# Kernel tuning notes

Measured on AMD Instinct MI355X. Metric: run time of the kernel, lower is better.

The kernel has to match this reference:

```python
import jax, jax.numpy as jnp
import numpy as np

H = 1024      # hidden_size
NH = 16       # num_heads
HD = H // NH  # head_dim
MLP_DIM = 4096
EPS = 1e-6


def setup_inputs() -> dict:
    key = jax.random.key(0)
    ks = jax.random.split(key, 16)
    B, S = 8, 1024
    s_in = 1.0 / np.sqrt(H)
    s_mlp = 1.0 / np.sqrt(MLP_DIM)
    return {
        "x": jax.random.normal(ks[0], (B, S, H), jnp.float32),
        "ln1_g": jnp.ones((H,), jnp.float32),
        "ln1_b": jnp.zeros((H,), jnp.float32),
        "Wq": jax.random.normal(ks[1], (H, H), jnp.float32) * s_in,
        "bq": jnp.zeros((H,), jnp.float32),
        "Wk": jax.random.normal(ks[2], (H, H), jnp.float32) * s_in,
        "bk": jnp.zeros((H,), jnp.float32),
        "Wv": jax.random.normal(ks[3], (H, H), jnp.float32) * s_in,
        "bv": jnp.zeros((H,), jnp.float32),
        "Wo": jax.random.normal(ks[4], (H, H), jnp.float32) * s_in,
        "bo": jnp.zeros((H,), jnp.float32),
        "ln2_g": jnp.ones((H,), jnp.float32),
        "ln2_b": jnp.zeros((H,), jnp.float32),
        "W1": jax.random.normal(ks[5], (H, MLP_DIM), jnp.float32) * s_in,
        "b1": jnp.zeros((MLP_DIM,), jnp.float32),
        "W2": jax.random.normal(ks[6], (MLP_DIM, H), jnp.float32) * s_mlp,
        "b2": jnp.zeros((H,), jnp.float32),
    }


def _layernorm(x, g, b):
    mu = jnp.mean(x, axis=-1, keepdims=True)
    var = jnp.mean(jnp.square(x - mu), axis=-1, keepdims=True)
    return (x - mu) * jax.lax.rsqrt(var + EPS) * g + b


def reference(x, ln1_g, ln1_b, Wq, bq, Wk, bk, Wv, bv, Wo, bo,
              ln2_g, ln2_b, W1, b1, W2, b2):
    B, S, _ = x.shape
    # pre-LN attention
    h = _layernorm(x, ln1_g, ln1_b)
    q = (h @ Wq + bq).reshape(B, S, NH, HD).transpose(0, 2, 1, 3)  # bhsd
    k = (h @ Wk + bk).reshape(B, S, NH, HD).transpose(0, 2, 1, 3)
    v = (h @ Wv + bv).reshape(B, S, NH, HD).transpose(0, 2, 1, 3)
    scale = HD ** -0.5
    scores = jnp.einsum('bhqd,bhkd->bhqk', q, k) * scale
    weights = jax.nn.softmax(scores, axis=-1)
    attended = jnp.einsum('bhqk,bhkd->bhqd', weights, v)
    attended = attended.transpose(0, 2, 1, 3).reshape(B, S, H)
    x = x + attended @ Wo + bo
    # pre-LN MLP
    h = _layernorm(x, ln2_g, ln2_b)
    h = jax.nn.gelu(h @ W1 + b1, approximate=False)
    x = x + h @ W2 + b2
    return x
```

## Files before the change

kernel.cpp:

```cpp
#include <hip/hip_runtime.h>

#define H_DIM 1024
#define NHEADS 16
#define HD 64
#define SEQ 1024
#define BATCH 8
#define ROWS (BATCH*SEQ)
#define MLPD 4096

typedef __bf16 bf16x8 __attribute__((ext_vector_type(8)));
typedef float f32x4 __attribute__((ext_vector_type(4)));

__device__ __forceinline__ unsigned short f2bf(float f) {
    unsigned u = __float_as_uint(f);
    unsigned r = u + 0x7FFFu + ((u >> 16) & 1u);
    return (unsigned short)(r >> 16);
}

__global__ void transpose_w(const float* __restrict__ in, unsigned short* __restrict__ out,
                            int K, int N)
{
    __shared__ float tile[32][33];
    const int n0 = blockIdx.x * 32, k0 = blockIdx.y * 32;
    const int tx = threadIdx.x, ty = threadIdx.y;
    #pragma unroll
    for (int i = ty; i < 32; i += 8)
        tile[i][tx] = in[(size_t)(k0 + i) * N + n0 + tx];
    __syncthreads();
    #pragma unroll
    for (int i = ty; i < 32; i += 8)
        out[(size_t)(n0 + i) * K + k0 + tx] = f2bf(tile[tx][i]);
}

__global__ void transpose_v(const unsigned short* __restrict__ in,
                            unsigned short* __restrict__ out)
{
    __shared__ unsigned short tile[32][33];
    const size_t base = (size_t)blockIdx.z * (SEQ * HD);
    const int d0 = blockIdx.x * 32, s0 = blockIdx.y * 32;
    const int tx = threadIdx.x, ty = threadIdx.y;
    #pragma unroll
    for (int i = ty; i < 32; i += 8)
        tile[i][tx] = in[base + (size_t)(s0 + i) * HD + d0 + tx];
    __syncthreads();
    const int fx = ((tx & 12) << 1) | ((tx & 16) >> 2) | (tx & 3);
    #pragma unroll
    for (int i = ty; i < 32; i += 8)
        out[base + (size_t)(d0 + i) * SEQ + s0 + fx] = tile[tx][i];
}

__global__ __launch_bounds__(256) void ln_kernel(const float* __restrict__ x,
    const float* __restrict__ g, const float* __restrict__ b,
    unsigned short* __restrict__ out)
{
    __shared__ float red[4];
    const int row = blockIdx.x;
    const int tid = threadIdx.x;
    const float4 v = *(const float4*)(x + (size_t)row * H_DIM + tid * 4);
    float s = v.x + v.y + v.z + v.w;
    #pragma unroll
    for (int off = 32; off >= 1; off >>= 1) s += __shfl_xor(s, off);
    if ((tid & 63) == 0) red[tid >> 6] = s;
    __syncthreads();
    const float mu = (red[0] + red[1] + red[2] + red[3]) * (1.0f / H_DIM);
    __syncthreads();
    const float dx = v.x - mu, dy = v.y - mu, dz = v.z - mu, dw = v.w - mu;
    float q = dx * dx + dy * dy + dz * dz + dw * dw;
    #pragma unroll
    for (int off = 32; off >= 1; off >>= 1) q += __shfl_xor(q, off);
    if ((tid & 63) == 0) red[tid >> 6] = q;
    __syncthreads();
    const float var = (red[0] + red[1] + red[2] + red[3]) * (1.0f / H_DIM);
    const float rstd = rsqrtf(var + 1e-6f);
    const float4 gv = *(const float4*)(g + tid * 4);
    const float4 bv = *(const float4*)(b + tid * 4);
    ushort4 o;
    o.x = f2bf(dx * rstd * gv.x + bv.x);
    o.y = f2bf(dy * rstd * gv.y + bv.y);
    o.z = f2bf(dz * rstd * gv.z + bv.z);
    o.w = f2bf(dw * rstd * gv.w + bv.w);
    *(ushort4*)(out + (size_t)row * H_DIM + tid * 4) = o;
}

template<int MODE>
__global__ __launch_bounds__(256) void gemm_dp(
    const unsigned short* __restrict__ A, const unsigned short* __restrict__ Bt,
    const float* __restrict__ bias0, const float* __restrict__ bias1,
    const float* __restrict__ bias2, const float* resid,
    float* outF, unsigned short* __restrict__ outH,
    int N, int K, int gn)
{
    __shared__ __align__(16) unsigned short As[128 * 64];
    __shared__ __align__(16) unsigned short Bs[128 * 64];

    const int tid = threadIdx.x, lane = tid & 63;
    const int w = tid >> 6;
    const int wm = w >> 1, wn = w & 1;

    const int nwg = gridDim.x;
    const int swzb = (blockIdx.x & 7) * (nwg >> 3) + (blockIdx.x >> 3);
    const int bm = swzb / gn, bn = swzb % gn;

    const int srow = tid >> 3;
    const int sc = (tid & 7) ^ (srow & 7);
    const unsigned short* Abase = A  + (size_t)(bm * 128) * K;
    const unsigned short* Bbase = Bt + (size_t)(bn * 128) * K;

    auto stage = [&](int kt) {
        const size_t kofs = (size_t)kt * 64 + sc * 8;
        #pragma unroll
        for (int q = 0; q < 4; ++q)
            __builtin_amdgcn_global_load_lds(
                (__attribute__((address_space(1))) void*)(Abase + (size_t)(q * 32 + srow) * K + kofs),
                (__attribute__((address_space(3))) void*)(&As[q * 2048 + tid * 8]), 16, 0, 0);
        #pragma unroll
        for (int q = 0; q < 4; ++q)
            __builtin_amdgcn_global_load_lds(
                (__attribute__((address_space(1))) void*)(Bbase + (size_t)(q * 32 + srow) * K + kofs),
                (__attribute__((address_space(3))) void*)(&Bs[q * 2048 + tid * 8]), 16, 0, 0);
    };

    const int lr = lane & 15, hk = lane >> 4;
    const int px0 = (hk ^ (lr & 7)) * 8;
    const int px1 = px0 ^ 32;
    const int arow = (wm * 64 + lr) * 64;
    const int brow = (wn * 64 + lr) * 64;

    f32x4 acc[4][4] = {};
    const int nkt = K >> 6;

    for (int t = 0; t < nkt; ++t) {
        stage(t);
        __syncthreads();

        const unsigned short* Ab = &As[arow];
        const unsigned short* Bb = &Bs[brow];

        bf16x8 a0[4], b0[4], a1[4], b1[4];
        #pragma unroll
        for (int i = 0; i < 4; ++i) { b0[i] = *(const bf16x8*)(Bb + i * 1024 + px0);
                                      a0[i] = *(const bf16x8*)(Ab + i * 1024 + px0); }
        #pragma unroll
        for (int i = 0; i < 4; ++i) { b1[i] = *(const bf16x8*)(Bb + i * 1024 + px1);
                                      a1[i] = *(const bf16x8*)(Ab + i * 1024 + px1); }
        __builtin_amdgcn_s_setprio(1);
        #pragma unroll
        for (int mi = 0; mi < 4; ++mi)
            #pragma unroll
            for (int ni = 0; ni < 4; ++ni)
                acc[mi][ni] = __builtin_amdgcn_mfma_f32_16x16x32_bf16(a0[mi], b0[ni], acc[mi][ni], 0, 0, 0);
        __builtin_amdgcn_s_setprio(0);
        __builtin_amdgcn_s_setprio(1);
        #pragma unroll
        for (int mi = 0; mi < 4; ++mi)
            #pragma unroll
            for (int ni = 0; ni < 4; ++ni)
                acc[mi][ni] = __builtin_amdgcn_mfma_f32_16x16x32_bf16(a1[mi], b1[ni], acc[mi][ni], 0, 0, 0);
        __builtin_amdgcn_s_setprio(0);
        __syncthreads();
    }

    #pragma unroll
    for (int mi = 0; mi < 4; ++mi) {
        #pragma unroll
        for (int ni = 0; ni < 4; ++ni) {
            const int gcol = bn * 128 + wn * 64 + ni * 16 + lr;
            #pragma unroll
            for (int r = 0; r < 4; ++r) {
                const int grow = bm * 128 + wm * 64 + mi * 16 + hk * 4 + r;
                if (MODE == 0) {
                    const int which = gcol >> 10;
                    const int col = gcol & 1023;
                    const float* bp = (which == 0) ? bias0 : (which == 1) ? bias1 : bias2;
                    const float v = acc[mi][ni][r] + bp[col];
                    const int b_ = grow >> 10, s_ = grow & 1023, h_ = col >> 6, d_ = col & 63;
                    outH[(size_t)which * (ROWS * 1024) +
                         (size_t)(b_ * NHEADS + h_) * 65536 + s_ * 64 + d_] = f2bf(v);
                } else if (MODE == 2) {
                    const float v = acc[mi][ni][r] + bias0[gcol];
                    const size_t idx = (size_t)grow * N + gcol;
                    outF[idx] = resid[idx] + v;
                }
            }
        }
    }
}

__global__ __launch_bounds__(512) void gemm8p(
    const unsigned short* __restrict__ A, const unsigned short* __restrict__ Bt,
    const float* __restrict__ bias, unsigned short* __restrict__ outH,
    int N, int K, int gn)
{
    __shared__ __align__(16) unsigned short As[2][16384];
    __shared__ __align__(16) unsigned short Bs[2][16384];

    const int tid = threadIdx.x, lane = tid & 63;
    const int w = tid >> 6;
    const int wm = w >> 2, wn = w & 3;

    const int nwg = gridDim.x;
    const int swzb = (blockIdx.x & 7) * (nwg >> 3) + (blockIdx.x >> 3);
    const int bm = swzb / gn, bn = swzb % gn;

    const int srow = tid >> 3;
    const int sc   = tid & 7;
    const unsigned short* Abase = A  + (size_t)(bm * 256) * K;
    const unsigned short* Bbase = Bt + (size_t)(bn * 256) * K;

    auto stageHalf = [&](int buf, int kt, int q) {
        const unsigned short* gb = (q >= 2) ? Bbase : Abase;
        unsigned short* lb = ((q >= 2) ? &Bs[buf][0] : &As[buf][0]) + (q & 1) * 8192;
        #pragma unroll
        for (int j = 0; j < 2; ++j) {
            const int row = srow + j * 64;
            __builtin_amdgcn_global_load_lds(
                (__attribute__((address_space(1))) void*)(gb
                    + (size_t)((q & 1) * 128 + row) * K + (size_t)kt * 64
                    + ((sc ^ (row & 7)) * 8)),
                (__attribute__((address_space(3))) void*)(lb + j * 4096 + tid * 8), 16, 0, 0);
        }
    };

    const int lr = lane & 15, hk = lane >> 4;
    const int swz0 = (hk ^ (lr & 7)) * 8;
    const int swz1 = swz0 ^ 32;

    f32x4 acc[8][4] = {};
    const int nkt = K >> 6;

    stageHalf(0, 0, 0); stageHalf(0, 0, 1); stageHalf(0, 0, 2); stageHalf(0, 0, 3);

    for (int t = 0; t < nkt; ++t) {
        const int cur = t & 1, nxt = cur ^ 1;
        bf16x8 bfr[4][2];
        #pragma unroll
        for (int q = 0; q < 4; ++q) {
            if (t + 1 < nkt) stageHalf(nxt, t + 1, q);
            if (q == 0) {
                if (t + 1 < nkt) asm volatile("s_waitcnt vmcnt(2)" ::: "memory");
                else             asm volatile("s_waitcnt vmcnt(0)" ::: "memory");
            }
            __builtin_amdgcn_s_barrier();
            asm volatile("" ::: "memory");
            if (q == 0) {
                const unsigned short* Bb = &Bs[cur][(wn >> 1) * 8192 + (wn & 1) * 4096];
                #pragma unroll
                for (int ni = 0; ni < 4; ++ni) {
                    const unsigned short* p = Bb + (ni * 16 + lr) * 64;
                    bfr[ni][0] = *(const bf16x8*)(p + swz0);
                    bfr[ni][1] = *(const bf16x8*)(p + swz1);
                }
            }
            bf16x8 afr[2][2];
            const unsigned short* Ab = &As[cur][wm * 8192];
            #pragma unroll
            for (int m2 = 0; m2 < 2; ++m2) {
                const unsigned short* p = Ab + ((q * 2 + m2) * 16 + lr) * 64;
                afr[m2][0] = *(const bf16x8*)(p + swz0);
                afr[m2][1] = *(const bf16x8*)(p + swz1);
            }
            __builtin_amdgcn_s_setprio(1);
            #pragma unroll
            for (int ks = 0; ks < 2; ++ks)
                #pragma unroll
                for (int m2 = 0; m2 < 2; ++m2)
                    #pragma unroll
                    for (int ni = 0; ni < 4; ++ni)
                        acc[q * 2 + m2][ni] = __builtin_amdgcn_mfma_f32_16x16x32_bf16(
                            afr[m2][ks], bfr[ni][ks], acc[q * 2 + m2][ni], 0, 0, 0);
            __builtin_amdgcn_s_setprio(0);
            __builtin_amdgcn_s_barrier();
            asm volatile("" ::: "memory");
        }
    }

    #pragma unroll
    for (int mf = 0; mf < 8; ++mf) {
        #pragma unroll
        for (int ni = 0; ni < 4; ++ni) {
            const int gcol = bn * 256 + wn * 64 + ni * 16 + lr;
            #pragma unroll
            for (int r = 0; r < 4; ++r) {
                const int grow = bm * 256 + wm * 128 + mf * 16 + hk * 4 + r;
                const float v = acc[mf][ni][r] + bias[gcol];
                const float t3 = fmaf(0.044715f * v * v, v, v);
                const float e  = __builtin_amdgcn_exp2f(-2.3022086f * t3);
                const float ge = v * __builtin_amdgcn_rcpf(1.0f + e);
                outH[(size_t)grow * N + gcol] = f2bf(ge);
            }
        }
    }
}

__global__ __launch_bounds__(256) void attn_kernel(const unsigned short* __restrict__ q,
    const unsigned short* __restrict__ k, const unsigned short* __restrict__ vT,
    unsigned short* __restrict__ out)
{
    __shared__ __align__(16) unsigned short Ks[2][4096];
    __shared__ __align__(16) unsigned short Vs[2][4096];
    const int tid = threadIdx.x, lane = tid & 63, w = tid >> 6;
    const int bh = blockIdx.y;
    const int q0 = blockIdx.x * 64;
    const size_t headBase = (size_t)bh * (SEQ * HD);

    const int qrow = q0 + w * 16 + (lane & 15);
    const unsigned short* qp = q + headBase + (size_t)qrow * HD + (lane >> 4) * 8;
    const bf16x8 qf0 = *(const bf16x8*)(qp);
    const bf16x8 qf1 = *(const bf16x8*)(qp + 32);

    float lacc = 0.f;
    f32x4 oacc[4] = {};

    const int srow = tid >> 3;
    const int swz  = ((tid & 7) ^ (srow & 7)) * 8;
    const int pc   = (lane >> 4) ^ (lane & 7);

    auto stage = [&](int buf, int kt) {
        #pragma unroll
        for (int s = 0; s < 2; ++s) {
            const unsigned short* gk = k  + headBase + (size_t)(kt + s * 32 + srow) * HD + swz;
            const unsigned short* gv = vT + headBase + (size_t)(s * 32 + srow) * SEQ + kt + swz;
            __builtin_amdgcn_global_load_lds((__attribute__((address_space(1))) void*)gk,
                (__attribute__((address_space(3))) void*)(&Ks[buf][s * 2048 + w * 512]), 16, 0, 0);
            __builtin_amdgcn_global_load_lds((__attribute__((address_space(1))) void*)gv,
                (__attribute__((address_space(3))) void*)(&Vs[buf][s * 2048 + w * 512]), 16, 0, 0);
        }
    };

    stage(0, 0);
    __syncthreads();

    const float C1 = 0.125f * 1.44269504f;
    const float C2 = -4.0f * 1.44269504f;

    for (int t = 0; t < 16; ++t) {
        const int cur = t & 1;
        if (t < 15) stage(cur ^ 1, (t + 1) * 64);

        const unsigned short* KB = &Ks[cur][0];
        const unsigned short* VB = &Vs[cur][0];

        f32x4 s4[4] = {};
        #pragma unroll
        for (int ni = 0; ni < 4; ++ni) {
            const unsigned short* pk = KB + (ni * 16 + (lane & 15)) * 64;
            s4[ni] = __builtin_amdgcn_mfma_f32_16x16x32_bf16(*(const bf16x8*)(pk + pc * 8),       qf0, s4[ni], 0, 0, 0);
            s4[ni] = __builtin_amdgcn_mfma_f32_16x16x32_bf16(*(const bf16x8*)(pk + (pc ^ 4) * 8), qf1, s4[ni], 0, 0, 0);
        }

        unsigned U[4][2];
        float ls = 0.f;
        #pragma unroll
        for (int ni = 0; ni < 4; ++ni) {
            const float p0 = __builtin_amdgcn_exp2f(fmaf(s4[ni][0], C1, C2));
            const float p1 = __builtin_amdgcn_exp2f(fmaf(s4[ni][1], C1, C2));
            const float p2 = __builtin_amdgcn_exp2f(fmaf(s4[ni][2], C1, C2));
            const float p3 = __builtin_amdgcn_exp2f(fmaf(s4[ni][3], C1, C2));
            ls += (p0 + p1) + (p2 + p3);
            asm("v_cvt_pk_bf16_f32 %0, %1, %2" : "=v"(U[ni][0]) : "v"(p0), "v"(p1));
            asm("v_cvt_pk_bf16_f32 %0, %1, %2" : "=v"(U[ni][1]) : "v"(p2), "v"(p3));
        }
        lacc += ls;

        union { unsigned u[4]; bf16x8 v; } W0, W1;
        W0.u[0] = U[0][0]; W0.u[1] = U[0][1]; W0.u[2] = U[1][0]; W0.u[3] = U[1][1];
        W1.u[0] = U[2][0]; W1.u[1] = U[2][1]; W1.u[2] = U[3][0]; W1.u[3] = U[3][1];

        #pragma unroll
        for (int nd = 0; nd < 4; ++nd) {
            const unsigned short* pv = VB + (nd * 16 + (lane & 15)) * 64;
            oacc[nd] = __builtin_amdgcn_mfma_f32_16x16x32_bf16(*(const bf16x8*)(pv + pc * 8),       W0.v, oacc[nd], 0, 0, 0);
            oacc[nd] = __builtin_amdgcn_mfma_f32_16x16x32_bf16(*(const bf16x8*)(pv + (pc ^ 4) * 8), W1.v, oacc[nd], 0, 0, 0);
        }

        __syncthreads();
    }

    float l = lacc;
    l += __shfl_xor(l, 16);
    l += __shfl_xor(l, 32);
    const float inv = 1.0f / l;

    const int b_ = bh >> 4, h_ = bh & 15;
    const int s_ = q0 + w * 16 + (lane & 15);
    const int hh = (lane >> 4) * 4;
    #pragma unroll
    for (int nd = 0; nd < 4; ++nd) {
        ushort4 o;
        o.x = f2bf(oacc[nd][0] * inv);
        o.y = f2bf(oacc[nd][1] * inv);
        o.z = f2bf(oacc[nd][2] * inv);
        o.w = f2bf(oacc[nd][3] * inv);
        *(ushort4*)(out + (size_t)(b_ * SEQ + s_) * H_DIM + h_ * 64 + nd * 16 + hh) = o;
    }
}

extern "C" void kernel_launch(void* const* d_in, const int* in_sizes, int n_in,
                              void* d_out, int out_size, void* d_ws, size_t ws_size,
                              hipStream_t stream)
{
    const float* x    = (const float*)d_in[0];
    const float* ln1g = (const float*)d_in[1];
    const float* ln1b = (const float*)d_in[2];
    const float* Wq   = (const float*)d_in[3];
    const float* bq   = (const float*)d_in[4];
    const float* Wk   = (const float*)d_in[5];
    const float* bk   = (const float*)d_in[6];
    const float* Wv   = (const float*)d_in[7];
    const float* bv   = (const float*)d_in[8];
    const float* Wo   = (const float*)d_in[9];
    const float* bo   = (const float*)d_in[10];
    const float* ln2g = (const float*)d_in[11];
    const float* ln2b = (const float*)d_in[12];
    const float* W1   = (const float*)d_in[13];
    const float* b1   = (const float*)d_in[14];
    const float* W2   = (const float*)d_in[15];
    const float* b2   = (const float*)d_in[16];
    float* out = (float*)d_out;

    char* ws = (char*)d_ws;
    const size_t MB = 1024 * 1024;
    unsigned short* h1  = (unsigned short*)(ws);
    unsigned short* qb  = (unsigned short*)(ws + 16 * MB);
    unsigned short* kb  = (unsigned short*)(ws + 32 * MB);
    unsigned short* vb  = (unsigned short*)(ws + 48 * MB);
    unsigned short* vTb = (unsigned short*)(ws + 64 * MB);
    unsigned short* mlp = (unsigned short*)(ws + 16 * MB);
    unsigned short* ao  = h1;
    unsigned short* WqT = (unsigned short*)(ws + 80 * MB);
    unsigned short* WkT = (unsigned short*)(ws + 82 * MB);
    unsigned short* WvT = (unsigned short*)(ws + 84 * MB);
    unsigned short* WoT = (unsigned short*)(ws + 86 * MB);
    unsigned short* W1T = (unsigned short*)(ws + 88 * MB);
    unsigned short* W2T = (unsigned short*)(ws + 96 * MB);

    const dim3 tb(32, 8);
    transpose_w<<<dim3(32, 32),  tb, 0, stream>>>(Wq, WqT, 1024, 1024);
    transpose_w<<<dim3(32, 32),  tb, 0, stream>>>(Wk, WkT, 1024, 1024);
    transpose_w<<<dim3(32, 32),  tb, 0, stream>>>(Wv, WvT, 1024, 1024);
    transpose_w<<<dim3(32, 32),  tb, 0, stream>>>(Wo, WoT, 1024, 1024);
    transpose_w<<<dim3(128, 32), tb, 0, stream>>>(W1, W1T, 1024, 4096);
    transpose_w<<<dim3(32, 128), tb, 0, stream>>>(W2, W2T, 4096, 1024);

    ln_kernel<<<ROWS, 256, 0, stream>>>(x, ln1g, ln1b, h1);

    gemm_dp<0><<<1536, 256, 0, stream>>>(h1, WqT, bq, bk, bv, nullptr, nullptr, qb, 3072, 1024, 24);

    transpose_v<<<dim3(2, 32, 128), tb, 0, stream>>>(vb, vTb);

    attn_kernel<<<dim3(16, 128), 256, 0, stream>>>(qb, kb, vTb, ao);

    gemm_dp<2><<<512, 256, 0, stream>>>(ao, WoT, bo, bo, bo, x, out, nullptr, 1024, 1024, 8);

    ln_kernel<<<ROWS, 256, 0, stream>>>(out, ln2g, ln2b, h1);

    gemm8p<<<512, 512, 0, stream>>>(h1, W1T, b1, mlp, 4096, 1024, 16);
    gemm_dp<2><<<512, 256, 0, stream>>>(mlp, W2T, b2, b2, b2, out, out, nullptr, 1024, 4096, 8);
}
```

Before: 395.8 us.

## Restructure MLP up-projection GEMM staging into two K-halves with finer waitcnt pipelining

```diff
diff --git a/kernel.cpp b/kernel.cpp
--- a/kernel.cpp
+++ b/kernel.cpp
@@ -180,19 +180,25 @@
                     const float v = acc[mi][ni][r] + bias0[gcol];
                     const size_t idx = (size_t)grow * N + gcol;
                     outF[idx] = resid[idx] + v;
+                } else {
+                    const float v = acc[mi][ni][r] + bias0[gcol];
+                    const float t3 = fmaf(0.044715f * v * v, v, v);
+                    const float e  = __builtin_amdgcn_exp2f(-2.3022086f * t3);
+                    const float ge = v * __builtin_amdgcn_rcpf(1.0f + e);
+                    outH[(size_t)grow * N + gcol] = f2bf(ge);
                 }
             }
         }
     }
 }
 
-__global__ __launch_bounds__(512) void gemm8p(
+__global__ __launch_bounds__(512) void gemm8k(
     const unsigned short* __restrict__ A, const unsigned short* __restrict__ Bt,
     const float* __restrict__ bias, unsigned short* __restrict__ outH,
     int N, int K, int gn)
 {
-    __shared__ __align__(16) unsigned short As[2][16384];
-    __shared__ __align__(16) unsigned short Bs[2][16384];
+    __shared__ __align__(16) unsigned short As[2][2][8192];
+    __shared__ __align__(16) unsigned short Bs[2][2][8192];
 
     const int tid = threadIdx.x, lane = tid & 63;
     const int w = tid >> 6;
@@ -202,72 +208,78 @@
     const int swzb = (blockIdx.x & 7) * (nwg >> 3) + (blockIdx.x >> 3);
     const int bm = swzb / gn, bn = swzb % gn;
 
-    const int srow = tid >> 3;
-    const int sc   = tid & 7;
     const unsigned short* Abase = A  + (size_t)(bm * 256) * K;
     const unsigned short* Bbase = Bt + (size_t)(bn * 256) * K;
 
-    auto stageHalf = [&](int buf, int kt, int q) {
-        const unsigned short* gb = (q >= 2) ? Bbase : Abase;
-        unsigned short* lb = ((q >= 2) ? &Bs[buf][0] : &As[buf][0]) + (q & 1) * 8192;
+    int srow[2], soff[2];
+    #pragma unroll
+    for (int j = 0; j < 2; ++j) {
+        const int slot = j * 512 + tid;
+        srow[j] = slot >> 2;
+        const int p = slot & 3;
+        soff[j] = (p ^ ((srow[j] >> 1) & 3)) * 8;
+    }
+
+    auto stageKH = [&](int buf, int kt, int s) {
         #pragma unroll
         for (int j = 0; j < 2; ++j) {
-            const int row = srow + j * 64;
+            const size_t off = (size_t)srow[j] * K + (size_t)kt * 64 + s * 32 + soff[j];
             __builtin_amdgcn_global_load_lds(
-                (__attribute__((address_space(1))) void*)(gb
-                    + (size_t)((q & 1) * 128 + row) * K + (size_t)kt * 64
-                    + ((sc ^ (row & 7)) * 8)),
-                (__attribute__((address_space(3))) void*)(lb + j * 4096 + tid * 8), 16, 0, 0);
+                (__attribute__((address_space(1))) void*)(Abase + off),
+                (__attribute__((address_space(3))) void*)(&As[buf][s][(j * 512 + tid) * 8]), 16, 0, 0);
+            __builtin_amdgcn_global_load_lds(
+                (__attribute__((address_space(1))) void*)(Bbase + off),
+                (__attribute__((address_space(3))) void*)(&Bs[buf][s][(j * 512 + tid) * 8]), 16, 0, 0);
         }
     };
 
     const int lr = lane & 15, hk = lane >> 4;
-    const int swz0 = (hk ^ (lr & 7)) * 8;
-    const int swz1 = swz0 ^ 32;
+    int aoff[8], boff[4];
+    #pragma unroll
+    for (int mf = 0; mf < 8; ++mf) {
+        const int R = wm * 128 + mf * 16 + lr;
+        aoff[mf] = R * 32 + ((hk ^ ((R >> 1) & 3)) * 8);
+    }
+    #pragma unroll
+    for (int nf = 0; nf < 4; ++nf) {
+        const int R = wn * 64 + nf * 16 + lr;
+        boff[nf] = R * 32 + ((hk ^ ((R >> 1) & 3)) * 8);
+    }
 
     f32x4 acc[8][4] = {};
     const int nkt = K >> 6;
 
-    stageHalf(0, 0, 0); stageHalf(0, 0, 1); stageHalf(0, 0, 2); stageHalf(0, 0, 3);
+    stageKH(0, 0, 0);
+    stageKH(0, 0, 1);
 
     for (int t = 0; t < nkt; ++t) {
-        const int cur = t & 1, nxt = cur ^ 1;
-        bf16x8 bfr[4][2];
-        #pragma unroll
-        for (int q = 0; q < 4; ++q) {
-            if (t + 1 < nkt) stageHalf(nxt, t + 1, q);
-            if (q == 0) {
-                if (t + 1 < nkt) asm volatile("s_waitcnt vmcnt(2)" ::: "memory");
-                else             asm volatile("s_waitcnt vmcnt(0)" ::: "memory");
+        const int buf = t & 1;
+        #pragma unroll
+        for (int s = 0; s < 2; ++s) {
+            if (t + 1 < nkt) {
+                stageKH(buf ^ 1, t + 1, s);
+                asm volatile("s_waitcnt vmcnt(8)" ::: "memory");
+            } else {
+                if (s == 0) asm volatile("s_waitcnt vmcnt(4)" ::: "memory");
+                else        asm volatile("s_waitcnt vmcnt(0)" ::: "memory");
             }
             __builtin_amdgcn_s_barrier();
             asm volatile("" ::: "memory");
-            if (q == 0) {
-                const unsigned short* Bb = &Bs[cur][(wn >> 1) * 8192 + (wn & 1) * 4096];
+
+            const unsigned short* Ar = &As[buf][s][0];
+            const unsigned short* Br = &Bs[buf][s][0];
+            bf16x8 af[8], bf[4];
+            #pragma unroll
+            for (int nf = 0; nf < 4; ++nf) bf[nf] = *(const bf16x8*)(Br + boff[nf]);
+            #pragma unroll
+            for (int mf = 0; mf < 8; ++mf) af[mf] = *(const bf16x8*)(Ar + aoff[mf]);
+
+            __builtin_amdgcn_s_setprio(1);
+            #pragma unroll
+            for (int mf = 0; mf < 8; ++mf)
                 #pragma unroll
-                for (int ni = 0; ni < 4; ++ni) {
-                    const unsigned short* p = Bb + (ni * 16 + lr) * 64;
-                    bfr[ni][0] = *(const bf16x8*)(p + swz0);
-                    bfr[ni][1] = *(const bf16x8*)(p + swz1);
-                }
-            }
-            bf16x8 afr[2][2];
-            const unsigned short* Ab = &As[cur][wm * 8192];
-            #pragma unroll
-            for (int m2 = 0; m2 < 2; ++m2) {
-                const unsigned short* p = Ab + ((q * 2 + m2) * 16 + lr) * 64;
-                afr[m2][0] = *(const bf16x8*)(p + swz0);
-                afr[m2][1] = *(const bf16x8*)(p + swz1);
-            }
-            __builtin_amdgcn_s_setprio(1);
-            #pragma unroll
-            for (int ks = 0; ks < 2; ++ks)
-                #pragma unroll
-                for (int m2 = 0; m2 < 2; ++m2)
-                    #pragma unroll
-                    for (int ni = 0; ni < 4; ++ni)
-                        acc[q * 2 + m2][ni] = __builtin_amdgcn_mfma_f32_16x16x32_bf16(
-                            afr[m2][ks], bfr[ni][ks], acc[q * 2 + m2][ni], 0, 0, 0);
+                for (int nf = 0; nf < 4; ++nf)
+                    acc[mf][nf] = __builtin_amdgcn_mfma_f32_16x16x32_bf16(af[mf], bf[nf], acc[mf][nf], 0, 0, 0);
             __builtin_amdgcn_s_setprio(0);
             __builtin_amdgcn_s_barrier();
             asm volatile("" ::: "memory");
@@ -277,12 +289,12 @@
     #pragma unroll
     for (int mf = 0; mf < 8; ++mf) {
         #pragma unroll
-        for (int ni = 0; ni < 4; ++ni) {
-            const int gcol = bn * 256 + wn * 64 + ni * 16 + lr;
+        for (int nf = 0; nf < 4; ++nf) {
+            const int gcol = bn * 256 + wn * 64 + nf * 16 + lr;
             #pragma unroll
             for (int r = 0; r < 4; ++r) {
                 const int grow = bm * 256 + wm * 128 + mf * 16 + hk * 4 + r;
-                const float v = acc[mf][ni][r] + bias[gcol];
+                const float v = acc[mf][nf][r] + bias[gcol];
                 const float t3 = fmaf(0.044715f * v * v, v, v);
                 const float e  = __builtin_amdgcn_exp2f(-2.3022086f * t3);
                 const float ge = v * __builtin_amdgcn_rcpf(1.0f + e);
@@ -454,6 +466,6 @@
 
     ln_kernel<<<ROWS, 256, 0, stream>>>(out, ln2g, ln2b, h1);
 
-    gemm8p<<<512, 512, 0, stream>>>(h1, W1T, b1, mlp, 4096, 1024, 16);
+    gemm8k<<<512, 512, 0, stream>>>(h1, W1T, b1, mlp, 4096, 1024, 16);
     gemm_dp<2><<<512, 256, 0, stream>>>(mlp, W2T, b2, b2, b2, out, out, nullptr, 1024, 4096, 8);
 }
```

After: 379.0 us. 1.04x faster.
